# Kernel optimization log

Measured on AMD Instinct MI355X. Metric: run time of the kernel, lower is better.

Reference implementation:

```python
import jax, jax.numpy as jnp
import numpy as np

B, N, D, H, MLP = 8, 1024, 1024, 16, 4096
DEPTH = D // H
EPS = 1e-6
INV_SQRT_DEPTH = 1.0 / np.sqrt(DEPTH).astype(np.float32)


def _linear_params(key, fan_in, fan_out):
    w = jax.random.normal(key, (fan_in, fan_out), dtype=jnp.float32) * 0.02
    b = jnp.zeros((fan_out,), dtype=jnp.float32)
    return w, b


def setup_inputs() -> dict:
    key = jax.random.key(0)
    ks = jax.random.split(key, 20)
    inp = {}
    inp['inputs'] = jax.random.normal(ks[0], (B, N, D), dtype=jnp.float32)
    inp['z'] = jax.random.normal(ks[1], (B, D), dtype=jnp.float32)
    # norm1 conditioning MLPs
    inp['n1_hw'], inp['n1_hb'] = _linear_params(ks[2], D, D)
    inp['n1_gw'], inp['n1_gb'] = _linear_params(ks[3], D, D)
    inp['n1_bw'], inp['n1_bb'] = _linear_params(ks[4], D, D)
    # attention
    inp['wq_w'], inp['wq_b'] = _linear_params(ks[5], D, D)
    inp['wk_w'], inp['wk_b'] = _linear_params(ks[6], D, D)
    inp['wv_w'], inp['wv_b'] = _linear_params(ks[7], D, D)
    inp['qa_w'], inp['qa_b'] = _linear_params(ks[8], D, H)
    inp['out_w'], inp['out_b'] = _linear_params(ks[9], D, D)
    # norm2 conditioning MLPs
    inp['n2_hw'], inp['n2_hb'] = _linear_params(ks[10], D, D)
    inp['n2_gw'], inp['n2_gb'] = _linear_params(ks[11], D, D)
    inp['n2_bw'], inp['n2_bb'] = _linear_params(ks[12], D, D)
    # MLP
    inp['mlp_w1'], inp['mlp_b1'] = _linear_params(ks[13], D, MLP)
    inp['mlp_w2'], inp['mlp_b2'] = _linear_params(ks[14], MLP, D)
    return inp


def _sm_norm(x, z, hw, hb, gw, gb, bw, bb):
    # LayerNorm over last dim, no affine
    mean = jnp.mean(x, axis=-1, keepdims=True)
    var = jnp.mean(jnp.square(x - mean), axis=-1, keepdims=True)
    xn = (x - mean) / jnp.sqrt(var + EPS)
    h = jax.nn.relu(z @ hw + hb)                 # [B, D]
    scale = (h @ gw + gb)[:, :, None]            # [B, D, 1]
    shift = (h @ bw + bb)[:, :, None]            # [B, D, 1]
    # broadcasts since N == D (as in the torch module)
    return xn * scale + shift


def _additive_attn(x, wq_w, wq_b, wk_w, wk_b, wv_w, wv_b, qa_w, qa_b, out_w, out_b):
    q = x @ wq_w + wq_b                          # [B, N, D]
    k = x @ wk_w + wk_b
    v = x @ wv_w + wv_b
    attn = jnp.transpose(q @ qa_w + qa_b, (0, 2, 1)) * INV_SQRT_DEPTH  # [B, H, N]
    attn = jax.nn.softmax(attn, axis=-1)
    qh = q.reshape(B, N, H, DEPTH).transpose(0, 2, 1, 3)  # [B, H, N, d]
    kh = k.reshape(B, N, H, DEPTH).transpose(0, 2, 1, 3)
    vh = v.reshape(B, N, H, DEPTH).transpose(0, 2, 1, 3)
    global_q = jnp.einsum('bhn,bhnd->bhd', attn, qh)[:, :, None, :]  # [B, H, 1, d]
    r = global_q * kh * vh                       # [B, H, N, d]
    r = r.transpose(0, 2, 1, 3).reshape(B, N, D)
    return r @ out_w + out_b, attn


def reference(inputs, z,
              n1_hw, n1_hb, n1_gw, n1_gb, n1_bw, n1_bb,
              wq_w, wq_b, wk_w, wk_b, wv_w, wv_b, qa_w, qa_b, out_w, out_b,
              n2_hw, n2_hb, n2_gw, n2_gb, n2_bw, n2_bb,
              mlp_w1, mlp_b1, mlp_w2, mlp_b2):
    x_norm1 = _sm_norm(inputs, z, n1_hw, n1_hb, n1_gw, n1_gb, n1_bw, n1_bb)
    attn_out, attn_maps = _additive_attn(x_norm1, wq_w, wq_b, wk_w, wk_b,
                                         wv_w, wv_b, qa_w, qa_b, out_w, out_b)
    attn_out = inputs + attn_out                 # dropout rate 0 -> identity
    x_norm2 = _sm_norm(attn_out, z, n2_hw, n2_hb, n2_gw, n2_gb, n2_bw, n2_bb)
    h = jax.nn.gelu(x_norm2 @ mlp_w1 + mlp_b1, approximate=False)
    mlp_out = h @ mlp_w2 + mlp_b2
    output = attn_out + mlp_out
    return output, attn_maps
```

## Files before the change

### kernel.cpp

```cpp
#include <hip/hip_runtime.h>
#include <math.h>


typedef __attribute__((ext_vector_type(8))) short short8;
typedef __attribute__((ext_vector_type(4))) float f32x4;

#define DEVI __device__ __forceinline__

DEVI unsigned short f2bf(float f) {
  union { float f; unsigned int u; } c; c.f = f;
  unsigned int r = c.u + 0x7fffu + ((c.u >> 16) & 1u);
  return (unsigned short)(r >> 16);
}
DEVI float bf2f(unsigned short u) {
  union { unsigned int u; float f; } c; c.u = ((unsigned int)u) << 16;
  return c.f;
}

DEVI void async16(const void* g, void* l) {
  __builtin_amdgcn_global_load_lds((const __attribute__((address_space(1))) void*)g,
                                   (__attribute__((address_space(3))) void*)l, 16, 0, 0);
}

__global__ void transpose_bf16_k(const float* __restrict__ in,
                                 unsigned short* __restrict__ out, int R, int C) {
  __shared__ float tile[32][33];
  const int c0 = blockIdx.x * 32, r0 = blockIdx.y * 32;
  const int tx = threadIdx.x, ty = threadIdx.y;
#pragma unroll
  for (int j = 0; j < 4; j++) {
    int r = r0 + ty + j * 8, c = c0 + tx;
    if (r < R && c < C) tile[ty + j * 8][tx] = in[(size_t)r * C + c];
  }
  __syncthreads();
#pragma unroll
  for (int j = 0; j < 4; j++) {
    int c = c0 + ty + j * 8, r = r0 + tx;
    if (c < C && r < R) out[(size_t)c * R + r] = f2bf(tile[tx][ty + j * 8]);
  }
}

__global__ void pad_bias_k(const float* __restrict__ qa_b, float* __restrict__ pad) {
  int t = threadIdx.x;
  pad[t] = (t < 16) ? qa_b[t] : 0.f;
}

__global__ void bias3_k(const float* __restrict__ b0, const float* __restrict__ b1,
                        const float* __restrict__ b2, float* __restrict__ out) {
  const int t = blockIdx.x * 256 + threadIdx.x;
  out[t] = (t < 1024) ? b0[t] : (t < 2048 ? b1[t - 1024] : b2[t - 2048]);
}

__global__ void zero_k(float4* __restrict__ p) {
  p[blockIdx.x * 256 + threadIdx.x] = float4{0.f, 0.f, 0.f, 0.f};
}

template <int NMAT>
__global__ __launch_bounds__(256) void skinny_k(const float* __restrict__ X,
                                                const float* __restrict__ W0,
                                                const float* __restrict__ W1,
                                                float* __restrict__ acc0,
                                                float* __restrict__ acc1) {
  const int tid = threadIdx.x;
  const int jt = blockIdx.x, kc = blockIdx.y;
  const int jl = tid & 63, kg = tid >> 6;
  const int jcol = jt * 64 + jl;
  __shared__ float xs[8][64];
  for (int i = tid; i < 512; i += 256) {
    const int b = i >> 6, kk = i & 63;
    xs[b][kk] = X[b * 1024 + kc * 64 + kk];
  }
  __syncthreads();
  float a0[8], a1[8];
#pragma unroll
  for (int b = 0; b < 8; b++) { a0[b] = 0.f; a1[b] = 0.f; }
#pragma unroll
  for (int kk = 0; kk < 16; kk++) {
    const int k = kg * 16 + kk;
    const float w0 = W0[(size_t)(kc * 64 + k) * 1024 + jcol];
#pragma unroll
    for (int b = 0; b < 8; b++) a0[b] += xs[b][k] * w0;
    if (NMAT == 2) {
      const float w1 = W1[(size_t)(kc * 64 + k) * 1024 + jcol];
#pragma unroll
      for (int b = 0; b < 8; b++) a1[b] += xs[b][k] * w1;
    }
  }
  __shared__ float red[256][9];
#pragma unroll
  for (int b = 0; b < 8; b++) red[tid][b] = a0[b];
  __syncthreads();
  if (tid < 64) {
#pragma unroll
    for (int b = 0; b < 8; b++) {
      const float s = red[tid][b] + red[tid + 64][b] + red[tid + 128][b] + red[tid + 192][b];
      atomicAdd(&acc0[b * 1024 + jcol], s);
    }
  }
  if (NMAT == 2) {
    __syncthreads();
#pragma unroll
    for (int b = 0; b < 8; b++) red[tid][b] = a1[b];
    __syncthreads();
    if (tid < 64) {
#pragma unroll
      for (int b = 0; b < 8; b++) {
        const float s = red[tid][b] + red[tid + 64][b] + red[tid + 128][b] + red[tid + 192][b];
        atomicAdd(&acc1[b * 1024 + jcol], s);
      }
    }
  }
}

__global__ void h_epi_k(const float* __restrict__ acc, const float* __restrict__ hb,
                        float* __restrict__ h) {
  const int i = blockIdx.x * 256 + threadIdx.x;
  h[i] = fmaxf(acc[i] + hb[i & 1023], 0.f);
}

__global__ __launch_bounds__(256) void ln_mod_k(const float* __restrict__ x,
                                                const float* __restrict__ s_acc,
                                                const float* __restrict__ t_acc,
                                                const float* __restrict__ gb,
                                                const float* __restrict__ bb,
                                                unsigned short* __restrict__ out) {
  const int lane = threadIdx.x & 63, wid = threadIdx.x >> 6;
  const size_t row = (size_t)blockIdx.x * 4 + wid;
  const int n = (int)(row & 1023);
  const float4* xr = (const float4*)(x + row * 1024);
  float4 v[4];
  float s = 0.f, ss = 0.f;
#pragma unroll
  for (int j = 0; j < 4; j++) {
    v[j] = xr[j * 64 + lane];
    s += v[j].x + v[j].y + v[j].z + v[j].w;
    ss += v[j].x * v[j].x + v[j].y * v[j].y + v[j].z * v[j].z + v[j].w * v[j].w;
  }
#pragma unroll
  for (int o = 32; o > 0; o >>= 1) { s += __shfl_xor(s, o); ss += __shfl_xor(ss, o); }
  const float mean = s * (1.f / 1024.f);
  const float var = ss * (1.f / 1024.f) - mean * mean;
  const float inv = rsqrtf(var + 1e-6f);
  const float scale = s_acc[row] + gb[n];
  const float shift = t_acc[row] + bb[n];
  const float sc = scale * inv;
  const float sh = shift - mean * sc;
#pragma unroll
  for (int j = 0; j < 4; j++) {
    ushort4 o4;
    o4.x = f2bf(v[j].x * sc + sh);
    o4.y = f2bf(v[j].y * sc + sh);
    o4.z = f2bf(v[j].z * sc + sh);
    o4.w = f2bf(v[j].w * sc + sh);
    *(ushort4*)(out + row * 1024 + (size_t)(j * 64 + lane) * 4) = o4;
  }
}

template <int EPI, int BM>
__global__ __launch_bounds__(512, 2) void gemm256(const unsigned short* __restrict__ A,
                                                  const unsigned short* __restrict__ BT,
                                                  const float* __restrict__ bias,
                                                  const float* __restrict__ resid,
                                                  void* __restrict__ Cout,
                                                  int M, int N, int K) {
  constexpr int WROWS = BM / 2;
  constexpr int MF = WROWS / 16;
  constexpr int ALOADS = (BM * 8) / 512;
  constexpr int NLOADS = ALOADS + 4;
  __shared__ unsigned short As[2][BM * 64];
  __shared__ unsigned short Bs[2][256 * 64];
  const int tid = threadIdx.x;
  const int lane = tid & 63, w = tid >> 6;
  const int wm = w >> 2, wn = w & 3;
  const int lr = lane & 15;
  const int g0 = lane >> 4;
  const size_t brow = (size_t)blockIdx.y * BM;
  const size_t bcol = (size_t)blockIdx.x * 256;
  const unsigned short* Ab = A + brow * (size_t)K;
  const unsigned short* Bb = BT + bcol * (size_t)K;
  const int NT = K >> 6;

  const f32x4 zero = {0.f, 0.f, 0.f, 0.f};
  f32x4 acc[MF][4];
#pragma unroll
  for (int m = 0; m < MF; m++)
#pragma unroll
    for (int n = 0; n < 4; n++) acc[m][n] = zero;

  auto stage = [&](int k0, int d) {
#pragma unroll
    for (int i = 0; i < ALOADS; i++) {
      const int c = i * 512 + tid;
      const int r = c >> 3, g = c & 7;
      const int gl = g ^ (r & 7);
      async16(Ab + (size_t)r * K + (k0 + gl * 8), &As[d][c * 8]);
    }
#pragma unroll
    for (int i = 0; i < 4; i++) {
      const int c = i * 512 + tid;
      const int r = c >> 3, g = c & 7;
      const int gl = g ^ (r & 7);
      async16(Bb + (size_t)r * K + (k0 + gl * 8), &Bs[d][c * 8]);
    }
  };

  stage(0, 0);
  stage(64, 1);
  if constexpr (NLOADS == 8) asm volatile("s_waitcnt vmcnt(8)" ::: "memory");
  else asm volatile("s_waitcnt vmcnt(6)" ::: "memory");
  __builtin_amdgcn_s_barrier();

  for (int t = 0; t < NT; ++t) {
    const unsigned short* as = As[t & 1];
    const unsigned short* bs = Bs[t & 1];
#pragma unroll
    for (int kk = 0; kk < 64; kk += 32) {
      const int gk = (kk >> 3) + g0;
      short8 bfrag[4];
#pragma unroll
      for (int nf = 0; nf < 4; nf++) {
        const int r = wn * 64 + nf * 16 + lr;
        bfrag[nf] = *(const short8*)&bs[r * 64 + ((gk ^ (r & 7)) << 3)];
      }
      __builtin_amdgcn_s_setprio(1);
#pragma unroll
      for (int mf = 0; mf < MF; mf++) {
        const int r = wm * WROWS + mf * 16 + lr;
        const short8 afrag = *(const short8*)&as[r * 64 + ((gk ^ (r & 7)) << 3)];
#pragma unroll
        for (int nf = 0; nf < 4; nf++)
          acc[mf][nf] = __builtin_amdgcn_mfma_f32_16x16x32_bf16(afrag, bfrag[nf], acc[mf][nf], 0, 0, 0);
      }
      __builtin_amdgcn_s_setprio(0);
    }
    asm volatile("" ::: "memory");
    __builtin_amdgcn_s_barrier();
    if (t + 2 < NT) {
      stage((t + 2) << 6, t & 1);
      if constexpr (NLOADS == 8) asm volatile("s_waitcnt vmcnt(8)" ::: "memory");
      else asm volatile("s_waitcnt vmcnt(6)" ::: "memory");
    } else {
      asm volatile("s_waitcnt vmcnt(0)" ::: "memory");
    }
    __builtin_amdgcn_s_barrier();
  }

  const int lc = lane & 15, lrow = (lane >> 4) * 4;
#pragma unroll
  for (int nf = 0; nf < 4; nf++) {
    const size_t col = bcol + wn * 64 + nf * 16 + lc;
    const float bv = bias[col];
#pragma unroll
    for (int mf = 0; mf < MF; mf++) {
#pragma unroll
      for (int j = 0; j < 4; j++) {
        const size_t row = brow + wm * WROWS + mf * 16 + lrow + j;
        float v = acc[mf][nf][j] + bv;
        if (EPI == 0) {
          ((unsigned short*)Cout)[(size_t)(col >> 10) * ((size_t)M << 10) + row * 1024 + (col & 1023)] = f2bf(v);
        } else if (EPI == 1) {
          v = 0.5f * v * (1.0f + erff(v * 0.70710678118654752f));
          ((unsigned short*)Cout)[row * (size_t)N + col] = f2bf(v);
        } else {
          const size_t idx = row * (size_t)N + col;
          ((float*)Cout)[idx] = v + resid[idx];
        }
      }
    }
  }
}

template <int EPI>
__global__ __launch_bounds__(256) void gemm_bf16(const unsigned short* __restrict__ A,
                                                 const unsigned short* __restrict__ BT,
                                                 const float* __restrict__ bias,
                                                 const float* __restrict__ resid,
                                                 void* __restrict__ Cout,
                                                 int M, int N, int K) {
  __shared__ unsigned short As[128 * 64];
  __shared__ unsigned short Bs[128 * 64];
  const int tid = threadIdx.x;
  const int lane = tid & 63, wid = tid >> 6;
  const int wr = wid >> 1, wc = wid & 1;
  const size_t brow = (size_t)blockIdx.y * 128;
  const size_t bcol = (size_t)blockIdx.x * 128;
  const unsigned short* Ab = A + brow * (size_t)K;
  const unsigned short* Bb = BT + bcol * (size_t)K;

  const f32x4 zero = {0.f, 0.f, 0.f, 0.f};
  f32x4 acc[4][4];
#pragma unroll
  for (int m = 0; m < 4; m++)
#pragma unroll
    for (int n = 0; n < 4; n++) acc[m][n] = zero;

  for (int k0 = 0; k0 < K; k0 += 64) {
#pragma unroll
    for (int i = 0; i < 4; i++) {
      const int eo = (i * 256 + tid) * 8;
      const int r = eo >> 6, c = eo & 63;
      async16(Ab + (size_t)r * K + (k0 + c), &As[eo]);
      async16(Bb + (size_t)r * K + (k0 + c), &Bs[eo]);
    }
    __syncthreads();
    const int lr = lane & 15, lk = (lane >> 4) * 8;
#pragma unroll
    for (int kk = 0; kk < 64; kk += 32) {
      short8 af[4], bfv[4];
#pragma unroll
      for (int m = 0; m < 4; m++)
        af[m] = *(const short8*)&As[(wr * 64 + m * 16 + lr) * 64 + kk + lk];
#pragma unroll
      for (int n = 0; n < 4; n++)
        bfv[n] = *(const short8*)&Bs[(wc * 64 + n * 16 + lr) * 64 + kk + lk];
#pragma unroll
      for (int m = 0; m < 4; m++)
#pragma unroll
        for (int n = 0; n < 4; n++)
          acc[m][n] = __builtin_amdgcn_mfma_f32_16x16x32_bf16(af[m], bfv[n], acc[m][n], 0, 0, 0);
    }
    __syncthreads();
  }

  const int lc = lane & 15, lr4 = (lane >> 4) * 4;
#pragma unroll
  for (int n = 0; n < 4; n++) {
    const size_t col = bcol + wc * 64 + n * 16 + lc;
    const float bv = bias[col];
#pragma unroll
    for (int m = 0; m < 4; m++) {
#pragma unroll
      for (int j = 0; j < 4; j++) {
        const size_t row = brow + wr * 64 + m * 16 + lr4 + j;
        const size_t idx = row * (size_t)N + col;
        ((float*)Cout)[idx] = acc[m][n][j] + bv;
      }
    }
  }
}

__global__ __launch_bounds__(256) void softmax_k(const float* __restrict__ logits,
                                                 float* __restrict__ attn) {
  const int tid = threadIdx.x;
  const int bh = blockIdx.x;
  const int b = bh >> 4, h = bh & 15;
  __shared__ float redm[4];
  __shared__ float reds[4];
  float vals[4];
#pragma unroll
  for (int j = 0; j < 4; j++) {
    const int n = j * 256 + tid;
    vals[j] = logits[((size_t)b * 1024 + n) * 128 + h] * 0.125f;
  }
  float m = fmaxf(fmaxf(vals[0], vals[1]), fmaxf(vals[2], vals[3]));
#pragma unroll
  for (int o = 32; o > 0; o >>= 1) m = fmaxf(m, __shfl_xor(m, o));
  if ((tid & 63) == 0) redm[tid >> 6] = m;
  __syncthreads();
  m = fmaxf(fmaxf(redm[0], redm[1]), fmaxf(redm[2], redm[3]));
  float e[4];
  float s = 0.f;
#pragma unroll
  for (int j = 0; j < 4; j++) { e[j] = expf(vals[j] - m); s += e[j]; }
#pragma unroll
  for (int o = 32; o > 0; o >>= 1) s += __shfl_xor(s, o);
  if ((tid & 63) == 0) reds[tid >> 6] = s;
  __syncthreads();
  s = reds[0] + reds[1] + reds[2] + reds[3];
  const float invs = 1.f / s;
#pragma unroll
  for (int j = 0; j < 4; j++)
    attn[(size_t)bh * 1024 + j * 256 + tid] = e[j] * invs;
}

__global__ __launch_bounds__(256) void global_q_k(const float* __restrict__ attn,
                                                  const unsigned short* __restrict__ Q,
                                                  float* __restrict__ gq) {
  const int tid = threadIdx.x;
  const int bh = blockIdx.x;
  const int b = bh >> 4, h = bh & 15;
  const int d = tid & 63, g = tid >> 6;
  const float* arow = attn + (size_t)bh * 1024;
  const unsigned short* qcol = Q + (size_t)b * 1024 * 1024 + h * 64 + d;
  float acc = 0.f;
  for (int n = g * 256; n < g * 256 + 256; n++)
    acc += arow[n] * bf2f(qcol[(size_t)n * 1024]);
  __shared__ float red[256];
  red[tid] = acc;
  __syncthreads();
  if (g == 0) gq[(size_t)bh * 64 + d] = red[d] + red[64 + d] + red[128 + d] + red[192 + d];
}

__global__ __launch_bounds__(256) void r_k(const unsigned short* __restrict__ Kb,
                                           const unsigned short* __restrict__ Vb,
                                           const float* __restrict__ gq,
                                           unsigned short* __restrict__ R) {
  const size_t i = ((size_t)blockIdx.x * 256 + threadIdx.x) * 8;
  const int col = (int)(i & 1023);
  const size_t b = i >> 20;
  const int h = col >> 6, dd = col & 63;
  const float* g = gq + ((b << 4) + h) * 64 + dd;
  short8 kv = *(const short8*)(Kb + i);
  short8 vv = *(const short8*)(Vb + i);
  short8 r;
#pragma unroll
  for (int j = 0; j < 8; j++) {
    float f = g[j] * bf2f((unsigned short)kv[j]) * bf2f((unsigned short)vv[j]);
    r[j] = (short)f2bf(f);
  }
  *(short8*)(R + i) = r;
}

extern "C" void kernel_launch(void* const* d_in, const int* in_sizes, int n_in,
                              void* d_out, int out_size, void* d_ws, size_t ws_size,
                              hipStream_t stream) {
  (void)in_sizes; (void)n_in; (void)out_size; (void)ws_size;
  const float* inputs = (const float*)d_in[0];
  const float* z      = (const float*)d_in[1];
  const float* n1_hw = (const float*)d_in[2];  const float* n1_hb = (const float*)d_in[3];
  const float* n1_gw = (const float*)d_in[4];  const float* n1_gb = (const float*)d_in[5];
  const float* n1_bw = (const float*)d_in[6];  const float* n1_bb = (const float*)d_in[7];
  const float* wq_w  = (const float*)d_in[8];  const float* wq_b  = (const float*)d_in[9];
  const float* wk_w  = (const float*)d_in[10]; const float* wk_b  = (const float*)d_in[11];
  const float* wv_w  = (const float*)d_in[12]; const float* wv_b  = (const float*)d_in[13];
  const float* qa_w  = (const float*)d_in[14]; const float* qa_b  = (const float*)d_in[15];
  const float* out_w = (const float*)d_in[16]; const float* out_b = (const float*)d_in[17];
  const float* n2_hw = (const float*)d_in[18]; const float* n2_hb = (const float*)d_in[19];
  const float* n2_gw = (const float*)d_in[20]; const float* n2_gb = (const float*)d_in[21];
  const float* n2_bw = (const float*)d_in[22]; const float* n2_bb = (const float*)d_in[23];
  const float* mlp_w1 = (const float*)d_in[24]; const float* mlp_b1 = (const float*)d_in[25];
  const float* mlp_w2 = (const float*)d_in[26]; const float* mlp_b2 = (const float*)d_in[27];

  const int M = 8192, D = 1024, MLPD = 4096;

  char* ws = (char*)d_ws;
  size_t o = 0;
  auto alloc = [&](size_t bytes) -> char* {
    char* p = ws + o;
    o += (bytes + 255) & ~(size_t)255;
    return p;
  };
  unsigned short* wqkvT = (unsigned short*)alloc((size_t)3 * D * D * 2);
  unsigned short* woT = (unsigned short*)alloc((size_t)D * D * 2);
  unsigned short* w1T = (unsigned short*)alloc((size_t)MLPD * D * 2);
  unsigned short* w2T = (unsigned short*)alloc((size_t)D * MLPD * 2);
  unsigned short* qaT = (unsigned short*)alloc((size_t)128 * D * 2);
  unsigned short* xn  = (unsigned short*)alloc((size_t)M * D * 2);
  char* big = alloc((size_t)M * MLPD * 2);
  unsigned short* Qb = (unsigned short*)big;
  unsigned short* Kb = (unsigned short*)(big + (size_t)M * D * 2);
  unsigned short* Vb = (unsigned short*)(big + (size_t)M * D * 4);
  float* logits      = (float*)(big + (size_t)M * D * 6);
  unsigned short* hbuf = (unsigned short*)big;
  float* cacc  = (float*)alloc(6 * 8192 * 4);
  float* accH1 = cacc;
  float* accS1 = cacc + 1 * 8192;
  float* accT1 = cacc + 2 * 8192;
  float* accH2 = cacc + 3 * 8192;
  float* accS2 = cacc + 4 * 8192;
  float* accT2 = cacc + 5 * 8192;
  float* h1     = (float*)alloc(8 * 1024 * 4);
  float* h2     = (float*)alloc(8 * 1024 * 4);
  float* gq     = (float*)alloc(8 * 16 * 64 * 4);
  float* qa_b_pad = (float*)alloc(128 * 4);
  float* qkvb    = (float*)alloc(3072 * 4);

  float* out0 = (float*)d_out;
  float* attn = (float*)d_out + (size_t)M * D;

  const dim3 tb(32, 8);
  hipLaunchKernelGGL(transpose_bf16_k, dim3(32, 32), tb, 0, stream, wq_w, wqkvT, D, D);
  hipLaunchKernelGGL(transpose_bf16_k, dim3(32, 32), tb, 0, stream, wk_w, wqkvT + (size_t)D * D, D, D);
  hipLaunchKernelGGL(transpose_bf16_k, dim3(32, 32), tb, 0, stream, wv_w, wqkvT + (size_t)2 * D * D, D, D);
  hipLaunchKernelGGL(transpose_bf16_k, dim3(32, 32), tb, 0, stream, out_w, woT, D, D);
  hipLaunchKernelGGL(transpose_bf16_k, dim3(128, 32), tb, 0, stream, mlp_w1, w1T, D, MLPD);
  hipLaunchKernelGGL(transpose_bf16_k, dim3(32, 128), tb, 0, stream, mlp_w2, w2T, MLPD, D);
  hipLaunchKernelGGL(transpose_bf16_k, dim3(1, 32), tb, 0, stream, qa_w, qaT, D, 16);
  hipLaunchKernelGGL(pad_bias_k, dim3(1), dim3(128), 0, stream, qa_b, qa_b_pad);
  hipLaunchKernelGGL(bias3_k, dim3(12), dim3(256), 0, stream, wq_b, wk_b, wv_b, qkvb);

  hipLaunchKernelGGL(zero_k, dim3(48), dim3(256), 0, stream, (float4*)cacc);
  hipLaunchKernelGGL(skinny_k<1>, dim3(16, 16), dim3(256), 0, stream, z, n1_hw, (const float*)nullptr, accH1, (float*)nullptr);
  hipLaunchKernelGGL(h_epi_k, dim3(32), dim3(256), 0, stream, accH1, n1_hb, h1);
  hipLaunchKernelGGL(skinny_k<2>, dim3(16, 16), dim3(256), 0, stream, h1, n1_gw, n1_bw, accS1, accT1);
  hipLaunchKernelGGL(skinny_k<1>, dim3(16, 16), dim3(256), 0, stream, z, n2_hw, (const float*)nullptr, accH2, (float*)nullptr);
  hipLaunchKernelGGL(h_epi_k, dim3(32), dim3(256), 0, stream, accH2, n2_hb, h2);
  hipLaunchKernelGGL(skinny_k<2>, dim3(16, 16), dim3(256), 0, stream, h2, n2_gw, n2_bw, accS2, accT2);

  hipLaunchKernelGGL(ln_mod_k, dim3(M / 4), dim3(256), 0, stream, inputs, accS1, accT1, n1_gb, n1_bb, xn);

  hipLaunchKernelGGL((gemm256<0, 256>), dim3(12, 32), dim3(512), 0, stream, xn, wqkvT, qkvb, (const float*)nullptr, (void*)Qb, M, 3072, D);

  hipLaunchKernelGGL(gemm_bf16<3>, dim3(1, 64), dim3(256), 0, stream, Qb, qaT, qa_b_pad, (const float*)nullptr, (void*)logits, M, 128, D);

  hipLaunchKernelGGL(softmax_k, dim3(128), dim3(256), 0, stream, logits, attn);

  hipLaunchKernelGGL(global_q_k, dim3(128), dim3(256), 0, stream, attn, Qb, gq);

  hipLaunchKernelGGL(r_k, dim3(M * D / 8 / 256), dim3(256), 0, stream, Kb, Vb, gq, Kb);

  hipLaunchKernelGGL((gemm256<2, 128>), dim3(4, 64), dim3(512), 0, stream, Kb, woT, out_b, inputs, (void*)out0, M, D, D);

  hipLaunchKernelGGL(ln_mod_k, dim3(M / 4), dim3(256), 0, stream, out0, accS2, accT2, n2_gb, n2_bb, xn);

  hipLaunchKernelGGL((gemm256<1, 256>), dim3(16, 32), dim3(512), 0, stream, xn, w1T, mlp_b1, (const float*)nullptr, (void*)hbuf, M, MLPD, D);

  hipLaunchKernelGGL((gemm256<2, 128>), dim3(4, 64), dim3(512), 0, stream, hbuf, w2T, mlp_b2, out0, (void*)out0, M, D, MLPD);
}
```

Measured before the change: 704.7 us.

## Stage bf16 GEMM epilogue through LDS and remap workgroups for L2 locality

For the bf16-output GEMM epilogues, the MFMA operands are swapped so each lane holds four consecutive columns. Results are packed and written into the reused LDS buffer with an XOR swizzle, then copied out as 16-byte coalesced row stores instead of scattered 2-byte stores. Workgroup IDs are also remapped in groups of 8 so that neighbouring blocks share A/B tiles in cache. This adds a __syncthreads and a reliance on the LDS tile fitting the output, and the remap assumes the block count is divisible by 8.

```diff
diff --git a/kernel.cpp b/kernel.cpp
--- a/kernel.cpp
+++ b/kernel.cpp
@@ -163,19 +163,24 @@
                                                   const float* __restrict__ resid,
                                                   void* __restrict__ Cout,
                                                   int M, int N, int K) {
+  constexpr bool SWAP = (EPI == 0 || EPI == 1);
   constexpr int WROWS = BM / 2;
   constexpr int MF = WROWS / 16;
   constexpr int ALOADS = (BM * 8) / 512;
   constexpr int NLOADS = ALOADS + 4;
-  __shared__ unsigned short As[2][BM * 64];
-  __shared__ unsigned short Bs[2][256 * 64];
+  __shared__ unsigned short lds[2 * BM * 64 + 2 * 256 * 64];
+  unsigned short* As0 = lds;
+  unsigned short* Bs0 = lds + 2 * BM * 64;
   const int tid = threadIdx.x;
   const int lane = tid & 63, w = tid >> 6;
   const int wm = w >> 2, wn = w & 3;
   const int lr = lane & 15;
   const int g0 = lane >> 4;
-  const size_t brow = (size_t)blockIdx.y * BM;
-  const size_t bcol = (size_t)blockIdx.x * 256;
+  const int nwg = gridDim.x * gridDim.y;
+  const int rb = blockIdx.y * gridDim.x + blockIdx.x;
+  const int sb = (rb & 7) * (nwg >> 3) + (rb >> 3);
+  const size_t brow = (size_t)(sb / gridDim.x) * BM;
+  const size_t bcol = (size_t)(sb % gridDim.x) * 256;
   const unsigned short* Ab = A + brow * (size_t)K;
   const unsigned short* Bb = BT + bcol * (size_t)K;
   const int NT = K >> 6;
@@ -193,14 +198,14 @@
       const int c = i * 512 + tid;
       const int r = c >> 3, g = c & 7;
       const int gl = g ^ (r & 7);
-      async16(Ab + (size_t)r * K + (k0 + gl * 8), &As[d][c * 8]);
+      async16(Ab + (size_t)r * K + (k0 + gl * 8), &As0[(size_t)d * BM * 64 + c * 8]);
     }
 #pragma unroll
     for (int i = 0; i < 4; i++) {
       const int c = i * 512 + tid;
       const int r = c >> 3, g = c & 7;
       const int gl = g ^ (r & 7);
-      async16(Bb + (size_t)r * K + (k0 + gl * 8), &Bs[d][c * 8]);
+      async16(Bb + (size_t)r * K + (k0 + gl * 8), &Bs0[(size_t)d * 256 * 64 + c * 8]);
     }
   };
 
@@ -211,8 +216,8 @@
   __builtin_amdgcn_s_barrier();
 
   for (int t = 0; t < NT; ++t) {
-    const unsigned short* as = As[t & 1];
-    const unsigned short* bs = Bs[t & 1];
+    const unsigned short* as = As0 + (size_t)(t & 1) * BM * 64;
+    const unsigned short* bs = Bs0 + (size_t)(t & 1) * 256 * 64;
 #pragma unroll
     for (int kk = 0; kk < 64; kk += 32) {
       const int gk = (kk >> 3) + g0;
@@ -228,8 +233,12 @@
         const int r = wm * WROWS + mf * 16 + lr;
         const short8 afrag = *(const short8*)&as[r * 64 + ((gk ^ (r & 7)) << 3)];
 #pragma unroll
-        for (int nf = 0; nf < 4; nf++)
-          acc[mf][nf] = __builtin_amdgcn_mfma_f32_16x16x32_bf16(afrag, bfrag[nf], acc[mf][nf], 0, 0, 0);
+        for (int nf = 0; nf < 4; nf++) {
+          if constexpr (SWAP)
+            acc[mf][nf] = __builtin_amdgcn_mfma_f32_16x16x32_bf16(bfrag[nf], afrag, acc[mf][nf], 0, 0, 0);
+          else
+            acc[mf][nf] = __builtin_amdgcn_mfma_f32_16x16x32_bf16(afrag, bfrag[nf], acc[mf][nf], 0, 0, 0);
+        }
       }
       __builtin_amdgcn_s_setprio(0);
     }
@@ -245,25 +254,59 @@
     __builtin_amdgcn_s_barrier();
   }
 
-  const int lc = lane & 15, lrow = (lane >> 4) * 4;
-#pragma unroll
-  for (int nf = 0; nf < 4; nf++) {
-    const size_t col = bcol + wn * 64 + nf * 16 + lc;
-    const float bv = bias[col];
-#pragma unroll
-    for (int mf = 0; mf < MF; mf++) {
-#pragma unroll
-      for (int j = 0; j < 4; j++) {
-        const size_t row = brow + wm * WROWS + mf * 16 + lrow + j;
-        float v = acc[mf][nf][j] + bv;
-        if (EPI == 0) {
-          ((unsigned short*)Cout)[(size_t)(col >> 10) * ((size_t)M << 10) + row * 1024 + (col & 1023)] = f2bf(v);
-        } else if (EPI == 1) {
-          v = 0.5f * v * (1.0f + erff(v * 0.70710678118654752f));
-          ((unsigned short*)Cout)[row * (size_t)N + col] = f2bf(v);
-        } else {
+  if constexpr (SWAP) {
+    unsigned short* cst = lds;
+    const int g4 = (lane >> 4) * 4;
+#pragma unroll
+    for (int nf = 0; nf < 4; nf++) {
+#pragma unroll
+      for (int mf = 0; mf < MF; mf++) {
+        const int row = wm * WROWS + mf * 16 + lr;
+        const int colb = wn * 64 + nf * 16 + g4;
+        const float4 bv = *(const float4*)&bias[bcol + colb];
+        float v[4];
+#pragma unroll
+        for (int j = 0; j < 4; j++) {
+          v[j] = acc[mf][nf][j] + (&bv.x)[j];
+          if (EPI == 1) v[j] = 0.5f * v[j] * (1.0f + erff(v[j] * 0.70710678118654752f));
+        }
+        ushort4 p;
+        p.x = f2bf(v[0]); p.y = f2bf(v[1]); p.z = f2bf(v[2]); p.w = f2bf(v[3]);
+        const int byo = row * 512 + ((colb * 2) ^ ((row & 7) << 4));
+        *(ushort4*)((char*)cst + byo) = p;
+      }
+    }
+    __syncthreads();
+    unsigned short* outp;
+    size_t ostride;
+    if (EPI == 0) {
+      outp = (unsigned short*)Cout + (size_t)(bcol >> 10) * ((size_t)M << 10) + (bcol & 1023);
+      ostride = 1024;
+    } else {
+      outp = (unsigned short*)Cout + bcol;
+      ostride = (size_t)N;
+    }
+#pragma unroll
+    for (int it = 0; it < BM / 16; it++) {
+      const int fl = it * 4096 + tid * 8;
+      const int row = fl >> 8, colu = fl & 255;
+      const int byo = row * 512 + ((colu * 2) ^ ((row & 7) << 4));
+      const short8 val = *(const short8*)((char*)cst + byo);
+      *(short8*)(outp + (size_t)(brow + row) * ostride + colu) = val;
+    }
+  } else {
+    const int lc = lane & 15, lrow = (lane >> 4) * 4;
+#pragma unroll
+    for (int nf = 0; nf < 4; nf++) {
+      const size_t col = bcol + wn * 64 + nf * 16 + lc;
+      const float bv = bias[col];
+#pragma unroll
+      for (int mf = 0; mf < MF; mf++) {
+#pragma unroll
+        for (int j = 0; j < 4; j++) {
+          const size_t row = brow + wm * WROWS + mf * 16 + lrow + j;
           const size_t idx = row * (size_t)N + col;
-          ((float*)Cout)[idx] = v + resid[idx];
+          ((float*)Cout)[idx] = acc[mf][nf][j] + bv + resid[idx];
         }
       }
     }
```

Result: faster. 667.7 us (-5.3%).
